# Kernel tuning notes

Hardware: AMD Instinct MI355X
Metric: run time of the kernel (lower is better)

## Reference

```python
import jax, jax.numpy as jnp
import numpy as np

N_FQK, N_FV, N_REL, N_VAL, N_KNOW = 512, 256, 128, 64, 256
TOPK_QK, TOPK_V, TOPK_REL, TOPK_VAL = 64, 32, 16, 3
FQK_END = N_FQK
FV_END = N_FQK + N_FV
REL_END = FV_END + N_REL
VAL_END = REL_END + N_VAL
TOTAL = VAL_END + N_KNOW


def setup_inputs() -> dict:
    key = jax.random.key(0)
    k1, k2, k3, k4, k5 = jax.random.split(key, 5)
    B, S, D, DS = 8, 4096, 1024, 64
    x = jax.random.normal(k1, (B, S, D), dtype=jnp.float32)
    importance = jax.random.uniform(k2, (B, S), dtype=jnp.float32)
    proj_w = jax.random.normal(k3, (DS, D), dtype=jnp.float32) * (1.0 / np.sqrt(D))
    proj_b = jax.random.normal(k4, (DS,), dtype=jnp.float32) * 0.01
    neuron_emb = jax.random.normal(k5, (TOTAL, DS), dtype=jnp.float32) * 0.02
    return {"x": x, "importance": importance, "proj_w": proj_w,
            "proj_b": proj_b, "neuron_emb": neuron_emb}


def _topk_sparsify(w, k):
    # keep top-k values per row, zero elsewhere
    vals, idx = jax.lax.top_k(w, k)
    B = w.shape[0]
    sparse = jnp.zeros_like(w).at[jnp.arange(B)[:, None], idx].set(vals)
    return sparse, idx


def reference(x, importance, proj_w, proj_b, neuron_emb):
    # shared projection + normalized neuron embeddings (eval: dropout off,
    # no excitability bonus)
    h = jnp.einsum('bsd,kd->bsk', x, proj_w) + proj_b          # [B,S,d_space]
    emb_n = neuron_emb / jnp.linalg.norm(neuron_emb, axis=-1, keepdims=True)
    all_logits = jnp.einsum('bsk,nk->bsn', h, emb_n)            # [B,S,TOTAL]

    def agg(logits):
        pref = jax.nn.softmax(logits, axis=-1)                  # [B,S,n]
        return jnp.einsum('bs,bsn->bn', importance, pref)

    w_qk = agg(all_logits[..., :FQK_END])
    _, idx_qk = jax.lax.top_k(w_qk, TOPK_QK)
    idx_qk = jnp.sort(idx_qk, axis=-1)

    w_v = agg(all_logits[..., FQK_END:FV_END])
    _, idx_v = jax.lax.top_k(w_v, TOPK_V)
    idx_v = jnp.sort(idx_v, axis=-1)

    rel_logits = all_logits[..., FV_END:REL_END]
    # relational_Q and relational_K use the same logits slice (eval mode)
    rel_dense_Q = agg(rel_logits)
    rel_dense_K = agg(rel_logits)
    rel_Q, _ = _topk_sparsify(rel_dense_Q, TOPK_REL)
    rel_K, _ = _topk_sparsify(rel_dense_K, TOPK_REL)

    val_dense = agg(all_logits[..., REL_END:VAL_END])
    val_w, _ = _topk_sparsify(val_dense, TOPK_VAL)

    return idx_qk, idx_v, rel_Q, rel_K, val_w
```

## Files before the change

### kernel.cpp

```cpp
#include <hip/hip_runtime.h>


typedef short short8 __attribute__((ext_vector_type(8)));
typedef float f32x4 __attribute__((ext_vector_type(4)));

__device__ __forceinline__ unsigned short f32_to_bf16(float f) {
  unsigned u = __float_as_uint(f);
  u += 0x7FFF + ((u >> 16) & 1);
  return (unsigned short)(u >> 16);
}
__device__ __forceinline__ float bf16_to_f32(unsigned short h) {
  return __uint_as_float(((unsigned)h) << 16);
}
__device__ __forceinline__ void split8(const float4& a0, const float4& a1,
                                       short8& hi, short8& lo) {
  float af[8] = {a0.x, a0.y, a0.z, a0.w, a1.x, a1.y, a1.z, a1.w};
#pragma unroll
  for (int j = 0; j < 8; ++j) {
    unsigned short h = f32_to_bf16(af[j]);
    hi[j] = (short)h;
    lo[j] = (short)f32_to_bf16(af[j] - bf16_to_f32(h));
  }
}
#define MFMA(a, b, c) __builtin_amdgcn_mfma_f32_16x16x32_bf16(a, b, c, 0, 0, 0)

__global__ __launch_bounds__(256) void k_prep(const float* __restrict__ pw,
                                              const float* __restrict__ emb,
                                              unsigned short* __restrict__ whi,
                                              unsigned short* __restrict__ wlo,
                                              unsigned short* __restrict__ ehi,
                                              unsigned short* __restrict__ elo,
                                              float* __restrict__ wg) {
  int tid = blockIdx.x * 256 + threadIdx.x;
  if (tid < 7680) wg[tid] = 0.f;
  for (int i = tid; i < 65536; i += gridDim.x * 256) {
    float v = pw[i];
    unsigned short h = f32_to_bf16(v);
    whi[i] = h;
    wlo[i] = f32_to_bf16(v - bf16_to_f32(h));
  }
  int wid = tid >> 6, lane = tid & 63;
  int nw = gridDim.x * 4;
  for (int n = wid; n < 960; n += nw) {
    float v = emb[n * 64 + lane];
    float s = v * v;
#pragma unroll
    for (int off = 1; off < 64; off <<= 1) s += __shfl_xor(s, off);
    float vn = v / sqrtf(s);
    unsigned short h = f32_to_bf16(vn);
    ehi[n * 64 + lane] = h;
    elo[n * 64 + lane] = f32_to_bf16(vn - bf16_to_f32(h));
  }
}

__global__ __launch_bounds__(256) void k_proj(const float* __restrict__ x,
                                              const unsigned short* __restrict__ whi,
                                              const unsigned short* __restrict__ wlo,
                                              const float* __restrict__ pb,
                                              unsigned short* __restrict__ hhi,
                                              unsigned short* __restrict__ hlo) {
  int tid = threadIdx.x, w = tid >> 6, lane = tid & 63;
  int q = lane >> 4, c = lane & 15;
  int m0 = blockIdx.x * 32;
  int nt = w;

  f32x4 acc[2];
  acc[0] = (f32x4){0.f, 0.f, 0.f, 0.f};
  acc[1] = (f32x4){0.f, 0.f, 0.f, 0.f};

  const float* ap0 = x + (size_t)(m0 + c) * 1024 + q * 8;
  const float* ap1 = x + (size_t)(m0 + 16 + c) * 1024 + q * 8;
  float4 a00 = *(const float4*)(ap0), a01 = *(const float4*)(ap0 + 4);
  float4 a10 = *(const float4*)(ap1), a11 = *(const float4*)(ap1 + 4);

  for (int ks = 0; ks < 32; ++ks) {
    float4 n00, n01, n10, n11;
    if (ks < 31) {
      n00 = *(const float4*)(ap0 + (ks + 1) * 32);
      n01 = *(const float4*)(ap0 + (ks + 1) * 32 + 4);
      n10 = *(const float4*)(ap1 + (ks + 1) * 32);
      n11 = *(const float4*)(ap1 + (ks + 1) * 32 + 4);
    }
    size_t boff = (size_t)(nt * 16 + c) * 1024 + ks * 32 + q * 8;
    short8 bhi = *(const short8*)(whi + boff);
    short8 blo = *(const short8*)(wlo + boff);
    short8 ahi[2], alo[2];
    split8(a00, a01, ahi[0], alo[0]);
    split8(a10, a11, ahi[1], alo[1]);
#pragma unroll
    for (int mt = 0; mt < 2; ++mt) {
      acc[mt] = MFMA(ahi[mt], bhi, acc[mt]);
      acc[mt] = MFMA(ahi[mt], blo, acc[mt]);
      acc[mt] = MFMA(alo[mt], bhi, acc[mt]);
    }
    if (ks < 31) { a00 = n00; a01 = n01; a10 = n10; a11 = n11; }
  }

  float bias = pb[nt * 16 + c];
#pragma unroll
  for (int mt = 0; mt < 2; ++mt) {
#pragma unroll
    for (int r = 0; r < 4; ++r) {
      float val = acc[mt][r] + bias;
      int row = m0 + mt * 16 + q * 4 + r;
      unsigned short h = f32_to_bf16(val);
      hhi[(size_t)row * 64 + nt * 16 + c] = h;
      hlo[(size_t)row * 64 + nt * 16 + c] = f32_to_bf16(val - bf16_to_f32(h));
    }
  }
}

__global__ __launch_bounds__(256) void k_agg(const unsigned short* __restrict__ hhi,
                                             const unsigned short* __restrict__ hlo,
                                             const unsigned short* __restrict__ ehi,
                                             const unsigned short* __restrict__ elo,
                                             const float* __restrict__ imp,
                                             float* __restrict__ wg) {
  __shared__ float zpart[4][32][4];
  __shared__ float coefL[32][4];
  int tid = threadIdx.x, w = tid >> 6, lane = tid & 63;
  int q = lane >> 4, c = lane & 15;
  int row0 = blockIdx.x * 32;
  int b = row0 >> 12;

  short8 Ahi[2][2], Alo[2][2];
#pragma unroll
  for (int mt = 0; mt < 2; ++mt)
#pragma unroll
    for (int ks = 0; ks < 2; ++ks) {
      size_t base = (size_t)(row0 + mt * 16 + c) * 64 + ks * 32 + q * 8;
      Ahi[mt][ks] = *(const short8*)(hhi + base);
      Alo[mt][ks] = *(const short8*)(hlo + base);
    }

  f32x4 zacc[2];
  zacc[0] = (f32x4){0.f, 0.f, 0.f, 0.f};
  zacc[1] = (f32x4){0.f, 0.f, 0.f, 0.f};
  int cur_seg = 0;
  for (int i = 0; i < 15; ++i) {
    int nt = w + 4 * i;
    int s = (nt < 32) ? 0 : (nt < 48) ? 1 : (nt < 56) ? 2 : 3;
    if (s != cur_seg) {
#pragma unroll
      for (int mt = 0; mt < 2; ++mt)
#pragma unroll
        for (int r = 0; r < 4; ++r) {
          float v = zacc[mt][r];
          v += __shfl_xor(v, 1); v += __shfl_xor(v, 2);
          v += __shfl_xor(v, 4); v += __shfl_xor(v, 8);
          if (c == 0) zpart[w][mt * 16 + q * 4 + r][cur_seg] = v;
          zacc[mt][r] = 0.f;
        }
      cur_seg = s;
    }
    size_t eb = (size_t)(nt * 16 + c) * 64 + q * 8;
    short8 bhi0 = *(const short8*)(ehi + eb), bhi1 = *(const short8*)(ehi + eb + 32);
    short8 blo0 = *(const short8*)(elo + eb), blo1 = *(const short8*)(elo + eb + 32);
#pragma unroll
    for (int mt = 0; mt < 2; ++mt) {
      f32x4 l = (f32x4){0.f, 0.f, 0.f, 0.f};
      l = MFMA(Ahi[mt][0], bhi0, l); l = MFMA(Ahi[mt][1], bhi1, l);
      l = MFMA(Ahi[mt][0], blo0, l); l = MFMA(Ahi[mt][1], blo1, l);
      l = MFMA(Alo[mt][0], bhi0, l); l = MFMA(Alo[mt][1], bhi1, l);
#pragma unroll
      for (int r = 0; r < 4; ++r) zacc[mt][r] += __expf(l[r]);
    }
  }
#pragma unroll
  for (int mt = 0; mt < 2; ++mt)
#pragma unroll
    for (int r = 0; r < 4; ++r) {
      float v = zacc[mt][r];
      v += __shfl_xor(v, 1); v += __shfl_xor(v, 2);
      v += __shfl_xor(v, 4); v += __shfl_xor(v, 8);
      if (c == 0) zpart[w][mt * 16 + q * 4 + r][cur_seg] = v;
    }
  __syncthreads();
  if (tid < 128) {
    int row = tid & 31, sg = tid >> 5;
    float Z = zpart[0][row][sg] + zpart[1][row][sg] + zpart[2][row][sg] + zpart[3][row][sg];
    coefL[row][sg] = imp[row0 + row] / Z;
  }
  __syncthreads();

  f32x4 cf[2];
  int cs2 = -1;
  for (int i = 0; i < 15; ++i) {
    int nt = w + 4 * i;
    int s = (nt < 32) ? 0 : (nt < 48) ? 1 : (nt < 56) ? 2 : 3;
    if (s != cs2) {
#pragma unroll
      for (int mt = 0; mt < 2; ++mt)
#pragma unroll
        for (int r = 0; r < 4; ++r) cf[mt][r] = coefL[mt * 16 + q * 4 + r][s];
      cs2 = s;
    }
    size_t eb = (size_t)(nt * 16 + c) * 64 + q * 8;
    short8 bhi0 = *(const short8*)(ehi + eb), bhi1 = *(const short8*)(ehi + eb + 32);
    short8 blo0 = *(const short8*)(elo + eb), blo1 = *(const short8*)(elo + eb + 32);
    float wsum = 0.f;
#pragma unroll
    for (int mt = 0; mt < 2; ++mt) {
      f32x4 l = (f32x4){0.f, 0.f, 0.f, 0.f};
      l = MFMA(Ahi[mt][0], bhi0, l); l = MFMA(Ahi[mt][1], bhi1, l);
      l = MFMA(Ahi[mt][0], blo0, l); l = MFMA(Ahi[mt][1], blo1, l);
      l = MFMA(Alo[mt][0], bhi0, l); l = MFMA(Alo[mt][1], bhi1, l);
#pragma unroll
      for (int r = 0; r < 4; ++r) wsum = fmaf(__expf(l[r]), cf[mt][r], wsum);
    }
    wsum += __shfl_xor(wsum, 16);
    wsum += __shfl_xor(wsum, 32);
    if (lane < 16) atomicAdd(&wg[b * 960 + nt * 16 + c], wsum);
  }
}

__global__ __launch_bounds__(256) void k_topk(const float* __restrict__ wg,
                                              float* __restrict__ out) {
  __shared__ float vals[512];
  __shared__ int flags[512];
  int blk = blockIdx.x;
  int b = blk >> 2, t = blk & 3;
  int tid = threadIdx.x;
  const int Ns[4] = {512, 256, 128, 64};
  const int Ks[4] = {64, 32, 16, 3};
  const int Off[4] = {0, 512, 768, 896};
  int N = Ns[t], K = Ks[t], off = Off[t];
  for (int n = tid; n < N; n += 256) vals[n] = wg[b * 960 + off + n];
  __syncthreads();
  for (int n = tid; n < N; n += 256) {
    float v = vals[n];
    int rank = 0;
    for (int m = 0; m < N; ++m) {
      float u = vals[m];
      rank += (u > v || (u == v && m < n)) ? 1 : 0;
    }
    flags[n] = (rank < K) ? 1 : 0;
  }
  __syncthreads();
  if (t <= 1) {
    if (tid < 64) {
      int base = 0;
      for (int ch = 0; ch < N; ch += 64) {
        int n = ch + tid;
        int f = flags[n];
        unsigned long long mask = __ballot(f);
        if (f) {
          int pos = base + __popcll(mask & ((1ull << tid) - 1ull));
          if (t == 0) out[b * 64 + pos] = (float)n;
          else out[512 + b * 32 + pos] = (float)n;
        }
        base += __popcll(mask);
      }
    }
  } else if (t == 2) {
    for (int n = tid; n < 128; n += 256) {
      float v = flags[n] ? vals[n] : 0.f;
      out[768 + b * 128 + n] = v;
      out[1792 + b * 128 + n] = v;
    }
  } else {
    for (int n = tid; n < 64; n += 256) {
      float v = flags[n] ? vals[n] : 0.f;
      out[2816 + b * 64 + n] = v;
    }
  }
}

extern "C" void kernel_launch(void* const* d_in, const int* in_sizes, int n_in,
                              void* d_out, int out_size, void* d_ws, size_t ws_size,
                              hipStream_t stream) {
  const float* x   = (const float*)d_in[0];
  const float* imp = (const float*)d_in[1];
  const float* pw  = (const float*)d_in[2];
  const float* pb  = (const float*)d_in[3];
  const float* emb = (const float*)d_in[4];
  float* out = (float*)d_out;

  char* ws = (char*)d_ws;
  unsigned short* hhi = (unsigned short*)(ws);
  unsigned short* hlo = (unsigned short*)(ws + 4194304);
  unsigned short* whi = (unsigned short*)(ws + 8388608);
  unsigned short* wlo = (unsigned short*)(ws + 8519680);
  unsigned short* ehi = (unsigned short*)(ws + 8650752);
  unsigned short* elo = (unsigned short*)(ws + 8773632);
  float*          wg  = (float*)(ws + 8896512);

  hipLaunchKernelGGL(k_prep, dim3(64), dim3(256), 0, stream, pw, emb, whi, wlo, ehi, elo, wg);
  hipLaunchKernelGGL(k_proj, dim3(1024), dim3(256), 0, stream, x, whi, wlo, pb, hhi, hlo);
  hipLaunchKernelGGL(k_agg,  dim3(1024), dim3(256), 0, stream, hhi, hlo, ehi, elo, imp, wg);
  hipLaunchKernelGGL(k_topk, dim3(32), dim3(256), 0, stream, wg, out);
}
```

Baseline: 349.1 us.

## Fuse projection and aggregation kernels with LDS-staged triple-buffered x loads

Merges k_proj and k_agg into one kernel so the projected h tile stays in shared memory (with XOR swizzle) and never goes through global memory. x tiles are loaded asynchronously into LDS with global_load_lds in a three-slot ring, paced by explicit waitcnt and barriers, and the hi/lo bf16 split now uses the packed v_cvt_pk_bf16_f32 instruction. Embedding loads in both aggregation passes are software-prefetched one iteration ahead. This removes the 8 MB h round trip and one launch, at the cost of more LDS and registers per block and fragile manual vmcnt bookkeeping.

```diff
diff --git a/kernel.cpp b/kernel.cpp
--- a/kernel.cpp
+++ b/kernel.cpp
@@ -3,6 +3,7 @@
 
 typedef short short8 __attribute__((ext_vector_type(8)));
 typedef float f32x4 __attribute__((ext_vector_type(4)));
+typedef unsigned int uint4v __attribute__((ext_vector_type(4)));
 
 __device__ __forceinline__ unsigned short f32_to_bf16(float f) {
   unsigned u = __float_as_uint(f);
@@ -12,17 +13,42 @@
 __device__ __forceinline__ float bf16_to_f32(unsigned short h) {
   return __uint_as_float(((unsigned)h) << 16);
 }
-__device__ __forceinline__ void split8(const float4& a0, const float4& a1,
-                                       short8& hi, short8& lo) {
-  float af[8] = {a0.x, a0.y, a0.z, a0.w, a1.x, a1.y, a1.z, a1.w};
-#pragma unroll
-  for (int j = 0; j < 8; ++j) {
-    unsigned short h = f32_to_bf16(af[j]);
-    hi[j] = (short)h;
-    lo[j] = (short)f32_to_bf16(af[j] - bf16_to_f32(h));
-  }
-}
+
+__device__ __forceinline__ unsigned cvt_pk_bf16(float a, float b) {
+  unsigned r;
+  asm("v_cvt_pk_bf16_f32 %0, %1, %2" : "=v"(r) : "v"(a), "v"(b));
+  return r;
+}
+
+__device__ __forceinline__ void split8v(const f32x4& v0, const f32x4& v1,
+                                        short8& hi, short8& lo) {
+  unsigned hp[4], lp[4];
+#pragma unroll
+  for (int j = 0; j < 4; ++j) {
+    float a = (j < 2) ? v0[2 * j] : v1[2 * j - 4];
+    float b = (j < 2) ? v0[2 * j + 1] : v1[2 * j - 3];
+    unsigned p = cvt_pk_bf16(a, b);
+    float ra = a - __uint_as_float(p << 16);
+    float rb = b - __uint_as_float(p & 0xFFFF0000u);
+    hp[j] = p;
+    lp[j] = cvt_pk_bf16(ra, rb);
+  }
+  hi = __builtin_bit_cast(short8, (uint4v){hp[0], hp[1], hp[2], hp[3]});
+  lo = __builtin_bit_cast(short8, (uint4v){lp[0], lp[1], lp[2], lp[3]});
+}
+
 #define MFMA(a, b, c) __builtin_amdgcn_mfma_f32_16x16x32_bf16(a, b, c, 0, 0, 0)
+
+typedef const __attribute__((address_space(1))) unsigned int guint;
+typedef __attribute__((address_space(3))) unsigned int luint;
+__device__ __forceinline__ void stage16(const float* g, float* l) {
+  __builtin_amdgcn_global_load_lds((guint*)g, (luint*)l, 16, 0, 0);
+}
+__device__ __forceinline__ void bar() {
+  asm volatile("" ::: "memory");
+  __builtin_amdgcn_s_barrier();
+  asm volatile("" ::: "memory");
+}
 
 __global__ __launch_bounds__(256) void k_prep(const float* __restrict__ pw,
                                               const float* __restrict__ emb,
@@ -53,128 +79,163 @@
   }
 }
 
-__global__ __launch_bounds__(256) void k_proj(const float* __restrict__ x,
-                                              const unsigned short* __restrict__ whi,
-                                              const unsigned short* __restrict__ wlo,
-                                              const float* __restrict__ pb,
-                                              unsigned short* __restrict__ hhi,
-                                              unsigned short* __restrict__ hlo) {
-  int tid = threadIdx.x, w = tid >> 6, lane = tid & 63;
-  int q = lane >> 4, c = lane & 15;
-  int m0 = blockIdx.x * 32;
-  int nt = w;
-
-  f32x4 acc[2];
-  acc[0] = (f32x4){0.f, 0.f, 0.f, 0.f};
-  acc[1] = (f32x4){0.f, 0.f, 0.f, 0.f};
-
-  const float* ap0 = x + (size_t)(m0 + c) * 1024 + q * 8;
-  const float* ap1 = x + (size_t)(m0 + 16 + c) * 1024 + q * 8;
-  float4 a00 = *(const float4*)(ap0), a01 = *(const float4*)(ap0 + 4);
-  float4 a10 = *(const float4*)(ap1), a11 = *(const float4*)(ap1 + 4);
-
-  for (int ks = 0; ks < 32; ++ks) {
-    float4 n00, n01, n10, n11;
-    if (ks < 31) {
-      n00 = *(const float4*)(ap0 + (ks + 1) * 32);
-      n01 = *(const float4*)(ap0 + (ks + 1) * 32 + 4);
-      n10 = *(const float4*)(ap1 + (ks + 1) * 32);
-      n11 = *(const float4*)(ap1 + (ks + 1) * 32 + 4);
-    }
-    size_t boff = (size_t)(nt * 16 + c) * 1024 + ks * 32 + q * 8;
-    short8 bhi = *(const short8*)(whi + boff);
-    short8 blo = *(const short8*)(wlo + boff);
-    short8 ahi[2], alo[2];
-    split8(a00, a01, ahi[0], alo[0]);
-    split8(a10, a11, ahi[1], alo[1]);
-#pragma unroll
-    for (int mt = 0; mt < 2; ++mt) {
-      acc[mt] = MFMA(ahi[mt], bhi, acc[mt]);
-      acc[mt] = MFMA(ahi[mt], blo, acc[mt]);
-      acc[mt] = MFMA(alo[mt], bhi, acc[mt]);
-    }
-    if (ks < 31) { a00 = n00; a01 = n01; a10 = n10; a11 = n11; }
-  }
-
-  float bias = pb[nt * 16 + c];
-#pragma unroll
-  for (int mt = 0; mt < 2; ++mt) {
-#pragma unroll
-    for (int r = 0; r < 4; ++r) {
-      float val = acc[mt][r] + bias;
-      int row = m0 + mt * 16 + q * 4 + r;
-      unsigned short h = f32_to_bf16(val);
-      hhi[(size_t)row * 64 + nt * 16 + c] = h;
-      hlo[(size_t)row * 64 + nt * 16 + c] = f32_to_bf16(val - bf16_to_f32(h));
-    }
-  }
-}
-
-__global__ __launch_bounds__(256) void k_agg(const unsigned short* __restrict__ hhi,
-                                             const unsigned short* __restrict__ hlo,
-                                             const unsigned short* __restrict__ ehi,
-                                             const unsigned short* __restrict__ elo,
-                                             const float* __restrict__ imp,
-                                             float* __restrict__ wg) {
+__global__ __launch_bounds__(256, 4) void k_main(
+    const float* __restrict__ x, const unsigned short* __restrict__ whi,
+    const unsigned short* __restrict__ wlo, const float* __restrict__ pb,
+    const unsigned short* __restrict__ ehi, const unsigned short* __restrict__ elo,
+    const float* __restrict__ imp, float* __restrict__ wg) {
+  __shared__ __align__(16) float xt[3][32][32];
+  __shared__ __align__(16) unsigned short hxh[32][64];
+  __shared__ __align__(16) unsigned short hxl[32][64];
   __shared__ float zpart[4][32][4];
   __shared__ float coefL[32][4];
-  int tid = threadIdx.x, w = tid >> 6, lane = tid & 63;
-  int q = lane >> 4, c = lane & 15;
-  int row0 = blockIdx.x * 32;
-  int b = row0 >> 12;
+
+  const int tid = threadIdx.x, w = tid >> 6, lane = tid & 63;
+  const int q = lane >> 4, c = lane & 15;
+  const int row0 = blockIdx.x * 32;
+  const int nt0 = w;
+
+  const int srow = tid >> 3;
+  const int scol = ((tid & 7) ^ (srow & 7)) * 4;
+  const float* sbase = x + (size_t)(row0 + srow) * 1024 + scol;
+  auto STAGEX = [&](int slot, int ks) {
+    stage16(sbase + ks * 32, &xt[slot][0][0] + (w << 8));
+  };
+
+  const unsigned short* bwh = whi + (size_t)(nt0 * 16 + c) * 1024 + q * 8;
+  const unsigned short* bwl = wlo + (size_t)(nt0 * 16 + c) * 1024 + q * 8;
+
+  f32x4 acc0 = {0.f, 0.f, 0.f, 0.f}, acc1 = {0.f, 0.f, 0.f, 0.f};
+
+  const unsigned sw = (unsigned)((c & 7) << 4);
+  const unsigned off1 = ((unsigned)(q * 32)) ^ sw;
+  const unsigned off2 = ((unsigned)(q * 32 + 16)) ^ sw;
+  const char* xby = (const char*)&xt[0][0][0] + (size_t)c * 128;
+
+  auto projstep = [&](int slot, short8 B_hi, short8 B_lo) {
+    const char* bp = xby + slot * 4096;
+    f32x4 a0 = *(const f32x4*)(bp + off1);
+    f32x4 a1 = *(const f32x4*)(bp + off2);
+    f32x4 a2 = *(const f32x4*)(bp + 2048 + off1);
+    f32x4 a3 = *(const f32x4*)(bp + 2048 + off2);
+    short8 ah, al;
+    split8v(a0, a1, ah, al);
+    acc0 = MFMA(ah, B_hi, acc0);
+    acc0 = MFMA(ah, B_lo, acc0);
+    acc0 = MFMA(al, B_hi, acc0);
+    split8v(a2, a3, ah, al);
+    acc1 = MFMA(ah, B_hi, acc1);
+    acc1 = MFMA(ah, B_lo, acc1);
+    acc1 = MFMA(al, B_hi, acc1);
+  };
+
+  STAGEX(0, 0);
+  STAGEX(1, 1);
+  short8 bh = *(const short8*)bwh;
+  short8 bl = *(const short8*)bwl;
+  short8 bh_n, bl_n;
+  int slot = 0;
+  for (int ks = 0; ks < 30; ++ks) {
+    int wslot = slot + 2; if (wslot >= 3) wslot -= 3;
+    STAGEX(wslot, ks + 2);
+    bh_n = *(const short8*)(bwh + (ks + 1) * 32);
+    bl_n = *(const short8*)(bwl + (ks + 1) * 32);
+    asm volatile("s_waitcnt vmcnt(6)" ::: "memory");
+    bar();
+    projstep(slot, bh, bl);
+    bar();
+    bh = bh_n; bl = bl_n;
+    ++slot; if (slot == 3) slot = 0;
+  }
+  bh_n = *(const short8*)(bwh + 31 * 32);
+  bl_n = *(const short8*)(bwl + 31 * 32);
+  asm volatile("s_waitcnt vmcnt(5)" ::: "memory");
+  bar();
+  projstep(slot, bh, bl);
+  bar();
+  ++slot; if (slot == 3) slot = 0;
+  asm volatile("s_waitcnt vmcnt(2)" ::: "memory");
+  bar();
+  projstep(slot, bh_n, bl_n);
+
+  float bias = pb[nt0 * 16 + c];
+#pragma unroll
+  for (int mt = 0; mt < 2; ++mt) {
+    f32x4 a = mt ? acc1 : acc0;
+#pragma unroll
+    for (int r = 0; r < 4; ++r) {
+      float val = a[r] + bias;
+      int row = mt * 16 + q * 4 + r;
+      unsigned colb = (unsigned)((nt0 * 16 + c) * 2);
+      unsigned o = (unsigned)(row * 128) + (colb ^ ((unsigned)(row & 7) << 4));
+      unsigned short h = f32_to_bf16(val);
+      *(unsigned short*)((char*)&hxh[0][0] + o) = h;
+      *(unsigned short*)((char*)&hxl[0][0] + o) = f32_to_bf16(val - bf16_to_f32(h));
+    }
+  }
+  __syncthreads();
 
   short8 Ahi[2][2], Alo[2][2];
 #pragma unroll
-  for (int mt = 0; mt < 2; ++mt)
-#pragma unroll
-    for (int ks = 0; ks < 2; ++ks) {
-      size_t base = (size_t)(row0 + mt * 16 + c) * 64 + ks * 32 + q * 8;
-      Ahi[mt][ks] = *(const short8*)(hhi + base);
-      Alo[mt][ks] = *(const short8*)(hlo + base);
-    }
-
-  f32x4 zacc[2];
-  zacc[0] = (f32x4){0.f, 0.f, 0.f, 0.f};
-  zacc[1] = (f32x4){0.f, 0.f, 0.f, 0.f};
+  for (int mt = 0; mt < 2; ++mt) {
+    int row = mt * 16 + c;
+    unsigned rs = (unsigned)((row & 7) << 4);
+#pragma unroll
+    for (int k2 = 0; k2 < 2; ++k2) {
+      unsigned o = (unsigned)(row * 128) + (((unsigned)(k2 * 64 + q * 16)) ^ rs);
+      Ahi[mt][k2] = *(const short8*)((const char*)&hxh[0][0] + o);
+      Alo[mt][k2] = *(const short8*)((const char*)&hxl[0][0] + o);
+    }
+  }
+
+  const size_t ebq = (size_t)c * 64 + q * 8;
+  auto ebase = [&](int i) { return (size_t)(w + 4 * i) * 1024 + ebq; };
+
+  f32x4 zacc0 = {0.f, 0.f, 0.f, 0.f}, zacc1 = {0.f, 0.f, 0.f, 0.f};
+  auto zflush = [&](int seg) {
+#pragma unroll
+    for (int mt = 0; mt < 2; ++mt)
+#pragma unroll
+      for (int r = 0; r < 4; ++r) {
+        float v = mt ? zacc1[r] : zacc0[r];
+        v += __shfl_xor(v, 1); v += __shfl_xor(v, 2);
+        v += __shfl_xor(v, 4); v += __shfl_xor(v, 8);
+        if (c == 0) zpart[w][mt * 16 + q * 4 + r][seg] = v;
+      }
+    zacc0 = (f32x4){0.f, 0.f, 0.f, 0.f};
+    zacc1 = (f32x4){0.f, 0.f, 0.f, 0.f};
+  };
+
+  short8 e0h, e1h, e0l, e1l, n0h, n1h, n0l, n1l;
+  {
+    size_t eb = ebase(0);
+    e0h = *(const short8*)(ehi + eb); e1h = *(const short8*)(ehi + eb + 32);
+    e0l = *(const short8*)(elo + eb); e1l = *(const short8*)(elo + eb + 32);
+  }
   int cur_seg = 0;
   for (int i = 0; i < 15; ++i) {
     int nt = w + 4 * i;
     int s = (nt < 32) ? 0 : (nt < 48) ? 1 : (nt < 56) ? 2 : 3;
-    if (s != cur_seg) {
-#pragma unroll
-      for (int mt = 0; mt < 2; ++mt)
-#pragma unroll
-        for (int r = 0; r < 4; ++r) {
-          float v = zacc[mt][r];
-          v += __shfl_xor(v, 1); v += __shfl_xor(v, 2);
-          v += __shfl_xor(v, 4); v += __shfl_xor(v, 8);
-          if (c == 0) zpart[w][mt * 16 + q * 4 + r][cur_seg] = v;
-          zacc[mt][r] = 0.f;
-        }
-      cur_seg = s;
-    }
-    size_t eb = (size_t)(nt * 16 + c) * 64 + q * 8;
-    short8 bhi0 = *(const short8*)(ehi + eb), bhi1 = *(const short8*)(ehi + eb + 32);
-    short8 blo0 = *(const short8*)(elo + eb), blo1 = *(const short8*)(elo + eb + 32);
+    if (s != cur_seg) { zflush(cur_seg); cur_seg = s; }
+    if (i < 14) {
+      size_t eb = ebase(i + 1);
+      n0h = *(const short8*)(ehi + eb); n1h = *(const short8*)(ehi + eb + 32);
+      n0l = *(const short8*)(elo + eb); n1l = *(const short8*)(elo + eb + 32);
+    }
 #pragma unroll
     for (int mt = 0; mt < 2; ++mt) {
-      f32x4 l = (f32x4){0.f, 0.f, 0.f, 0.f};
-      l = MFMA(Ahi[mt][0], bhi0, l); l = MFMA(Ahi[mt][1], bhi1, l);
-      l = MFMA(Ahi[mt][0], blo0, l); l = MFMA(Ahi[mt][1], blo1, l);
-      l = MFMA(Alo[mt][0], bhi0, l); l = MFMA(Alo[mt][1], bhi1, l);
-#pragma unroll
-      for (int r = 0; r < 4; ++r) zacc[mt][r] += __expf(l[r]);
-    }
-  }
-#pragma unroll
-  for (int mt = 0; mt < 2; ++mt)
-#pragma unroll
-    for (int r = 0; r < 4; ++r) {
-      float v = zacc[mt][r];
-      v += __shfl_xor(v, 1); v += __shfl_xor(v, 2);
-      v += __shfl_xor(v, 4); v += __shfl_xor(v, 8);
-      if (c == 0) zpart[w][mt * 16 + q * 4 + r][cur_seg] = v;
-    }
+      f32x4 l = {0.f, 0.f, 0.f, 0.f};
+      l = MFMA(Ahi[mt][0], e0h, l); l = MFMA(Ahi[mt][1], e1h, l);
+      l = MFMA(Ahi[mt][0], e0l, l); l = MFMA(Ahi[mt][1], e1l, l);
+      l = MFMA(Alo[mt][0], e0h, l); l = MFMA(Alo[mt][1], e1h, l);
+#pragma unroll
+      for (int r = 0; r < 4; ++r) {
+        if (mt == 0) zacc0[r] += __expf(l[r]); else zacc1[r] += __expf(l[r]);
+      }
+    }
+    e0h = n0h; e1h = n1h; e0l = n0l; e1l = n1l;
+  }
+  zflush(cur_seg);
   __syncthreads();
   if (tid < 128) {
     int row = tid & 31, sg = tid >> 5;
@@ -183,34 +244,45 @@
   }
   __syncthreads();
 
-  f32x4 cf[2];
+  const int bIdx = row0 >> 12;
+  f32x4 cf0, cf1;
   int cs2 = -1;
+  {
+    size_t eb = ebase(0);
+    e0h = *(const short8*)(ehi + eb); e1h = *(const short8*)(ehi + eb + 32);
+    e0l = *(const short8*)(elo + eb); e1l = *(const short8*)(elo + eb + 32);
+  }
   for (int i = 0; i < 15; ++i) {
     int nt = w + 4 * i;
     int s = (nt < 32) ? 0 : (nt < 48) ? 1 : (nt < 56) ? 2 : 3;
     if (s != cs2) {
 #pragma unroll
-      for (int mt = 0; mt < 2; ++mt)
-#pragma unroll
-        for (int r = 0; r < 4; ++r) cf[mt][r] = coefL[mt * 16 + q * 4 + r][s];
+      for (int r = 0; r < 4; ++r) {
+        cf0[r] = coefL[q * 4 + r][s];
+        cf1[r] = coefL[16 + q * 4 + r][s];
+      }
       cs2 = s;
     }
-    size_t eb = (size_t)(nt * 16 + c) * 64 + q * 8;
-    short8 bhi0 = *(const short8*)(ehi + eb), bhi1 = *(const short8*)(ehi + eb + 32);
-    short8 blo0 = *(const short8*)(elo + eb), blo1 = *(const short8*)(elo + eb + 32);
+    if (i < 14) {
+      size_t eb = ebase(i + 1);
+      n0h = *(const short8*)(ehi + eb); n1h = *(const short8*)(ehi + eb + 32);
+      n0l = *(const short8*)(elo + eb); n1l = *(const short8*)(elo + eb + 32);
+    }
     float wsum = 0.f;
 #pragma unroll
     for (int mt = 0; mt < 2; ++mt) {
-      f32x4 l = (f32x4){0.f, 0.f, 0.f, 0.f};
-      l = MFMA(Ahi[mt][0], bhi0, l); l = MFMA(Ahi[mt][1], bhi1, l);
-      l = MFMA(Ahi[mt][0], blo0, l); l = MFMA(Ahi[mt][1], blo1, l);
-      l = MFMA(Alo[mt][0], bhi0, l); l = MFMA(Alo[mt][1], bhi1, l);
-#pragma unroll
-      for (int r = 0; r < 4; ++r) wsum = fmaf(__expf(l[r]), cf[mt][r], wsum);
+      f32x4 l = {0.f, 0.f, 0.f, 0.f};
+      l = MFMA(Ahi[mt][0], e0h, l); l = MFMA(Ahi[mt][1], e1h, l);
+      l = MFMA(Ahi[mt][0], e0l, l); l = MFMA(Ahi[mt][1], e1l, l);
+      l = MFMA(Alo[mt][0], e0h, l); l = MFMA(Alo[mt][1], e1h, l);
+#pragma unroll
+      for (int r = 0; r < 4; ++r)
+        wsum = fmaf(__expf(l[r]), mt ? cf1[r] : cf0[r], wsum);
     }
     wsum += __shfl_xor(wsum, 16);
     wsum += __shfl_xor(wsum, 32);
-    if (lane < 16) atomicAdd(&wg[b * 960 + nt * 16 + c], wsum);
+    if (lane < 16) atomicAdd(&wg[bIdx * 960 + nt * 16 + c], wsum);
+    e0h = n0h; e1h = n1h; e0l = n0l; e1l = n1l;
   }
 }
 
@@ -277,16 +349,13 @@
   float* out = (float*)d_out;
 
   char* ws = (char*)d_ws;
-  unsigned short* hhi = (unsigned short*)(ws);
-  unsigned short* hlo = (unsigned short*)(ws + 4194304);
-  unsigned short* whi = (unsigned short*)(ws + 8388608);
-  unsigned short* wlo = (unsigned short*)(ws + 8519680);
-  unsigned short* ehi = (unsigned short*)(ws + 8650752);
-  unsigned short* elo = (unsigned short*)(ws + 8773632);
-  float*          wg  = (float*)(ws + 8896512);
+  unsigned short* whi = (unsigned short*)(ws);
+  unsigned short* wlo = (unsigned short*)(ws + 131072);
+  unsigned short* ehi = (unsigned short*)(ws + 262144);
+  unsigned short* elo = (unsigned short*)(ws + 385024);
+  float*          wg  = (float*)(ws + 507904);
 
   hipLaunchKernelGGL(k_prep, dim3(64), dim3(256), 0, stream, pw, emb, whi, wlo, ehi, elo, wg);
-  hipLaunchKernelGGL(k_proj, dim3(1024), dim3(256), 0, stream, x, whi, wlo, pb, hhi, hlo);
-  hipLaunchKernelGGL(k_agg,  dim3(1024), dim3(256), 0, stream, hhi, hlo, ehi, elo, imp, wg);
+  hipLaunchKernelGGL(k_main, dim3(1024), dim3(256), 0, stream, x, whi, wlo, pb, ehi, elo, imp, wg);
   hipLaunchKernelGGL(k_topk, dim3(32), dim3(256), 0, stream, wg, out);
 }
```

Result: faster. 301.2 us (-13.7%).
